# Kernel optimization log

Measured on AMD Instinct MI355X. Metric: run time of the kernel, lower is better.

## Reference

```python
import jax, jax.numpy as jnp
import numpy as np

EMBED = 768
HEADS = 12
HEAD_DIM = EMBED // HEADS
HIDDEN = 4 * EMBED
B, N = 8, 1024
EPS = 1e-5


def layernorm(x, g, b):
    mu = jnp.mean(x, axis=-1, keepdims=True)
    var = jnp.var(x, axis=-1, keepdims=True)
    return (x - mu) * jax.lax.rsqrt(var + EPS) * g + b


def setup_inputs() -> dict:
    key = jax.random.key(0)
    ks = jax.random.split(key, 8)
    s_qkv = 1.0 / np.sqrt(EMBED)
    s_fc1 = 1.0 / np.sqrt(EMBED)
    s_fc2 = 1.0 / np.sqrt(HIDDEN)
    return {
        "x": jax.random.normal(ks[0], (B, N, EMBED), dtype=jnp.float32),
        "ln1_g": jnp.ones((EMBED,), jnp.float32),
        "ln1_b": jnp.zeros((EMBED,), jnp.float32),
        "qkv_w": jax.random.uniform(ks[1], (3 * EMBED, EMBED), jnp.float32, -s_qkv, s_qkv),
        "qkv_b": jnp.zeros((3 * EMBED,), jnp.float32),
        "proj_w": jax.random.uniform(ks[2], (EMBED, EMBED), jnp.float32, -s_qkv, s_qkv),
        "proj_b": jnp.zeros((EMBED,), jnp.float32),
        "ln2_g": jnp.ones((EMBED,), jnp.float32),
        "ln2_b": jnp.zeros((EMBED,), jnp.float32),
        "fc1_w": jax.random.uniform(ks[3], (HIDDEN, EMBED), jnp.float32, -s_fc1, s_fc1),
        "fc1_b": jnp.zeros((HIDDEN,), jnp.float32),
        "fc2_w": jax.random.uniform(ks[4], (EMBED, HIDDEN), jnp.float32, -s_fc2, s_fc2),
        "fc2_b": jnp.zeros((EMBED,), jnp.float32),
    }


def reference(x, ln1_g, ln1_b, qkv_w, qkv_b, proj_w, proj_b,
              ln2_g, ln2_b, fc1_w, fc1_b, fc2_w, fc2_b):
    b, n, d = x.shape
    # --- attention sublayer ---
    h = layernorm(x, ln1_g, ln1_b)
    qkv = h @ qkv_w.T + qkv_b                      # [b,n,3d]
    qkv = qkv.reshape(b, n, 3, HEADS, HEAD_DIM).transpose(2, 0, 3, 1, 4)
    q, k, v = qkv[0], qkv[1], qkv[2]               # [b,h,n,hd]
    scores = jnp.einsum('bhqd,bhkd->bhqk', q, k) * (HEAD_DIM ** -0.5)
    attn = jax.nn.softmax(scores, axis=-1)
    ctx = jnp.einsum('bhqk,bhkd->bhqd', attn, v)   # [b,h,n,hd]
    ctx = ctx.transpose(0, 2, 1, 3).reshape(b, n, d)
    x = x + (ctx @ proj_w.T + proj_b)
    # --- MLP sublayer ---
    h = layernorm(x, ln2_g, ln2_b)
    h = jax.nn.gelu(h @ fc1_w.T + fc1_b, approximate=False)
    x = x + (h @ fc2_w.T + fc2_b)
    return x
```

## Files before the change

### kernel.cpp

```cpp
#include <hip/hip_runtime.h>
#include <cstdint>

typedef __bf16 bf16_t;
typedef __attribute__((ext_vector_type(8))) __bf16 bf16x8;
typedef __attribute__((ext_vector_type(4))) __bf16 bf16x4;
typedef __attribute__((ext_vector_type(4))) float f32x4;

#define MFMA16(a, b, c) __builtin_amdgcn_mfma_f32_16x16x32_bf16((a), (b), (c), 0, 0, 0)

#define GLOAD16(g, l) __builtin_amdgcn_global_load_lds(                      \
    (const __attribute__((address_space(1))) void*)(g),                      \
    (__attribute__((address_space(3))) void*)(l), 16, 0, 0)

__device__ inline float gelu_f(float v) {
    const float u = v + 0.044715f * v * v * v;
    return v / (1.0f + exp2f(-2.3022038f * u));
}

__global__ __launch_bounds__(256) void cvt4_kernel(const float* __restrict__ s0, bf16_t* __restrict__ d0,
                                                   const float* __restrict__ s1, bf16_t* __restrict__ d1,
                                                   const float* __restrict__ s2, bf16_t* __restrict__ d2,
                                                   const float* __restrict__ s3, bf16_t* __restrict__ d3) {
    const int blk = blockIdx.x;
    const float* s; bf16_t* d; int base;
    if (blk < 864)       { s = s0; d = d0; base = blk; }
    else if (blk < 1152) { s = s1; d = d1; base = blk - 864; }
    else if (blk < 2304) { s = s2; d = d2; base = blk - 1152; }
    else                 { s = s3; d = d3; base = blk - 2304; }
    const int i = (base * 256 + threadIdx.x) * 8;
    const float4* sp = (const float4*)(s + i);
    float4 a = sp[0], b = sp[1];
    bf16x8 o;
    o[0] = (bf16_t)a.x; o[1] = (bf16_t)a.y; o[2] = (bf16_t)a.z; o[3] = (bf16_t)a.w;
    o[4] = (bf16_t)b.x; o[5] = (bf16_t)b.y; o[6] = (bf16_t)b.z; o[7] = (bf16_t)b.w;
    *(bf16x8*)(d + i) = o;
}

__global__ __launch_bounds__(256) void ln_kernel(const float* __restrict__ x,
                                                 const float* __restrict__ gw,
                                                 const float* __restrict__ bw,
                                                 bf16_t* __restrict__ out) {
    const int row  = blockIdx.x * 4 + (threadIdx.x >> 6);
    const int lane = threadIdx.x & 63;
    const float4* xr = (const float4*)(x + (long)row * 768);
    float4 v[3];
    float s = 0.f, q = 0.f;
#pragma unroll
    for (int j = 0; j < 3; ++j) {
        v[j] = xr[j * 64 + lane];
        s += v[j].x + v[j].y + v[j].z + v[j].w;
        q += v[j].x * v[j].x + v[j].y * v[j].y + v[j].z * v[j].z + v[j].w * v[j].w;
    }
#pragma unroll
    for (int off = 32; off > 0; off >>= 1) {
        s += __shfl_xor(s, off);
        q += __shfl_xor(q, off);
    }
    const float mu = s * (1.0f / 768.0f);
    const float rs = rsqrtf(q * (1.0f / 768.0f) - mu * mu + 1e-5f);
#pragma unroll
    for (int j = 0; j < 3; ++j) {
        float4 g4 = ((const float4*)gw)[j * 64 + lane];
        float4 b4 = ((const float4*)bw)[j * 64 + lane];
        bf16x4 o;
        o[0] = (bf16_t)((v[j].x - mu) * rs * g4.x + b4.x);
        o[1] = (bf16_t)((v[j].y - mu) * rs * g4.y + b4.y);
        o[2] = (bf16_t)((v[j].z - mu) * rs * g4.z + b4.z);
        o[3] = (bf16_t)((v[j].w - mu) * rs * g4.w + b4.w);
        *(bf16x4*)(out + (long)row * 768 + (j * 64 + lane) * 4) = o;
    }
}

template <int MODE, int NC, int RPX>
__global__ __launch_bounds__(256) void gemm_bt(const bf16_t* __restrict__ A,
                                               const bf16_t* __restrict__ Bw,
                                               const float* __restrict__ bias,
                                               bf16_t* __restrict__ outb,
                                               bf16_t* __restrict__ o1,
                                               bf16_t* __restrict__ o2,
                                               int Nn, int K,
                                               const float* __restrict__ resf,
                                               float* __restrict__ outf) {
    __shared__ __align__(16) char smem[3 * (128 * 32 + 128 * 32) * 2];
    bf16_t* As = (bf16_t*)smem;
    bf16_t* Bs = (bf16_t*)(smem + 3 * 128 * 32 * 2);
    const int id = blockIdx.x;
    const int xcd = id & 7, sblk = id >> 3;
    const int tn = (sblk % NC) * 128;
    const int tm = (xcd * RPX + sblk / NC) * 128;
    const int w = threadIdx.x >> 6, l = threadIdx.x & 63;
    const int quad = l >> 4, r16 = l & 15;
    const int wm = (w >> 1) * 64, wn = (w & 1) * 64;
    f32x4 acc[4][4] = {};
    const bf16_t* ga = A  + (long)(tm + w * 32 + (l >> 2)) * K + (l & 3) * 8;
    const bf16_t* gb = Bw + (long)(tn + w * 32 + (l >> 2)) * K + (l & 3) * 8;
    const int lw = w * 1024;
    const int NK = K >> 5;

    auto issue = [&](int t) {
        const bf16_t* gan = ga + t * 32;
        const bf16_t* gbn = gb + t * 32;
        bf16_t* ab = As + (t % 3) * 4096;
        bf16_t* bb = Bs + (t % 3) * 4096;
        GLOAD16(gan,          ab + lw);
        GLOAD16(gan + 16 * K, ab + lw + 512);
        GLOAD16(gbn,          bb + lw);
        GLOAD16(gbn + 16 * K, bb + lw + 512);
    };
    auto compute = [&](int t) {
        const bf16_t* ab = As + (t % 3) * 4096;
        const bf16_t* bb = Bs + (t % 3) * 4096;
        bf16x8 af[4], bfr[4];
#pragma unroll
        for (int i = 0; i < 4; ++i) {
            af[i]  = *(const bf16x8*)&ab[(wm + i * 16 + r16) * 32 + quad * 8];
            bfr[i] = *(const bf16x8*)&bb[(wn + i * 16 + r16) * 32 + quad * 8];
        }
#pragma unroll
        for (int i = 0; i < 4; ++i)
#pragma unroll
            for (int j = 0; j < 4; ++j)
                acc[i][j] = MFMA16(af[i], bfr[j], acc[i][j]);
    };

    issue(0);
    issue(1);
    for (int t = 0; t < NK - 1; ++t) {
        asm volatile("s_waitcnt vmcnt(4)" ::: "memory");
        __builtin_amdgcn_s_barrier();
        if (t + 2 < NK) issue(t + 2);
        compute(t);
    }
    asm volatile("s_waitcnt vmcnt(0)" ::: "memory");
    __builtin_amdgcn_s_barrier();
    compute(NK - 1);

    __syncthreads();
    if (MODE == 3) {
        float* tf = (float*)smem + w * 16 * 68;
#pragma unroll
        for (int i = 0; i < 4; ++i) {
#pragma unroll
            for (int j = 0; j < 4; ++j) {
                const float bv = bias[tn + wn + j * 16 + r16];
#pragma unroll
                for (int rr = 0; rr < 4; ++rr)
                    tf[(quad * 4 + rr) * 68 + j * 16 + r16] = acc[i][j][rr] + bv;
            }
            const int grow = tm + wm + i * 16 + (l >> 2);
#pragma unroll
            for (int it = 0; it < 4; ++it) {
                const int gcol = tn + wn + (l & 3) * 4 + it * 16;
                f32x4 vv = *(const f32x4*)&tf[(l >> 2) * 68 + (l & 3) * 4 + it * 16];
                const float4 rv = *(const float4*)(resf + (long)grow * Nn + gcol);
                float4 ov;
                ov.x = rv.x + vv[0]; ov.y = rv.y + vv[1];
                ov.z = rv.z + vv[2]; ov.w = rv.w + vv[3];
                *(float4*)(outf + (long)grow * Nn + gcol) = ov;
            }
        }
        return;
    }
    bf16_t* tw = (bf16_t*)smem + w * 16 * 72;
    if (MODE == 0) {
        const int sect = (tn + wn) / 768;
        const int cwb  = tn + wn - sect * 768;
        const int h    = cwb >> 6;
        if (sect == 2) {
#pragma unroll
            for (int i = 0; i < 4; ++i) {
                const int r0 = tm + wm + i * 16 + quad * 4;
                const int b = r0 >> 10, n0 = r0 & 1023;
#pragma unroll
                for (int j = 0; j < 4; ++j) {
                    const int d = j * 16 + r16;
                    const float bv = bias[tn + wn + j * 16 + r16];
                    bf16_t* dst = o2 + ((long)(b * 12 + h) * 64 + d) * 1024;
#pragma unroll
                    for (int rr = 0; rr < 4; ++rr) {
                        const int nn = n0 + rr;
                        const int c = ((nn & 15) << 3) | ((nn >> 4) & 7);
                        dst[(nn & 0x380) + c] = (bf16_t)(acc[i][j][rr] + bv);
                    }
                }
            }
        } else {
            bf16_t* dstbuf = (sect == 0 ? outb : o1);
#pragma unroll
            for (int i = 0; i < 4; ++i) {
#pragma unroll
                for (int j = 0; j < 4; ++j) {
                    const float bv = bias[tn + wn + j * 16 + r16];
#pragma unroll
                    for (int rr = 0; rr < 4; ++rr)
                        tw[(quad * 4 + rr) * 72 + j * 16 + r16] = (bf16_t)(acc[i][j][rr] + bv);
                }
                const int tok = tm + wm + i * 16 + (l >> 2);
                const int b = tok >> 10, n0 = tok & 1023;
                const long base = (long)(b * 12 + h) * 65536 + (long)n0 * 64;
#pragma unroll
                for (int it = 0; it < 2; ++it) {
                    bf16x8 vv = *(const bf16x8*)&tw[(l >> 2) * 72 + (l & 3) * 8 + it * 32];
                    *(bf16x8*)(dstbuf + base + (l & 3) * 8 + it * 32) = vv;
                }
            }
        }
    } else {
#pragma unroll
        for (int i = 0; i < 4; ++i) {
#pragma unroll
            for (int j = 0; j < 4; ++j) {
                const float bv = bias[tn + wn + j * 16 + r16];
#pragma unroll
                for (int rr = 0; rr < 4; ++rr)
                    tw[(quad * 4 + rr) * 72 + j * 16 + r16] = (bf16_t)gelu_f(acc[i][j][rr] + bv);
            }
            const int grow = tm + wm + i * 16 + (l >> 2);
#pragma unroll
            for (int it = 0; it < 2; ++it) {
                bf16x8 vv = *(const bf16x8*)&tw[(l >> 2) * 72 + (l & 3) * 8 + it * 32];
                *(bf16x8*)(outb + (long)grow * Nn + tn + wn + (l & 3) * 8 + it * 32) = vv;
            }
        }
    }
}

__global__ __launch_bounds__(256, 3) void attn_kernel(const bf16_t* __restrict__ qh,
                                                      const bf16_t* __restrict__ kh,
                                                      const bf16_t* __restrict__ vt,
                                                      bf16_t* __restrict__ ctx) {
    __shared__ __align__(16) bf16_t Ks[128 * 72];
    __shared__ __align__(16) bf16_t Vt[64 * 136];
    __shared__ __align__(16) bf16_t Ps[4 * 16 * 136];
    const int w = threadIdx.x >> 6, l = threadIdx.x & 63;
    const int quad = l >> 4, r16 = l & 15;
    const int bh = blockIdx.x, qt = blockIdx.y;
    const bf16_t* qp = qh + (long)bh * 65536;
    const bf16_t* kp = kh + (long)bh * 65536;
    const bf16_t* vp = vt + (long)bh * 65536;
    const int q0 = qt * 128 + w * 32;
    const float SC = 0.18033688011f;

    bf16x8 qf[2][2];
#pragma unroll
    for (int mt = 0; mt < 2; ++mt)
#pragma unroll
        for (int kq = 0; kq < 2; ++kq)
            qf[mt][kq] = *(const bf16x8*)(qp + (long)(q0 + mt * 16 + r16) * 64 + kq * 32 + quad * 8);

    float lsum[2][4] = {};
    f32x4 oacc[2][4] = {};
    bf16_t* pw = Ps + w * 16 * 136;

    bf16x8 kpre[4], vpre[4];
#pragma unroll
    for (int c = 0; c < 4; ++c) {
        const int cc = threadIdx.x + c * 256;
        kpre[c] = *(const bf16x8*)(kp + (long)(cc >> 3) * 64 + (cc & 7) * 8);
        vpre[c] = *(const bf16x8*)(vp + (long)(cc >> 4) * 1024 + (cc & 15) * 8);
    }

    for (int kt = 0; kt < 8; ++kt) {
        __syncthreads();
#pragma unroll
        for (int c = 0; c < 4; ++c) {
            const int cc = threadIdx.x + c * 256;
            *(bf16x8*)&Ks[(cc >> 3) * 72 + (cc & 7) * 8] = kpre[c];
            *(bf16x8*)&Vt[(cc >> 4) * 136 + (cc & 15) * 8] = vpre[c];
        }
        __syncthreads();
        if (kt < 7) {
            const int kb = (kt + 1) * 128;
#pragma unroll
            for (int c = 0; c < 4; ++c) {
                const int cc = threadIdx.x + c * 256;
                kpre[c] = *(const bf16x8*)(kp + (long)(kb + (cc >> 3)) * 64 + (cc & 7) * 8);
                vpre[c] = *(const bf16x8*)(vp + (long)(cc >> 4) * 1024 + kb + (cc & 15) * 8);
            }
        }

#pragma unroll
        for (int mt = 0; mt < 2; ++mt) {
            f32x4 s[8] = {};
#pragma unroll
            for (int nt = 0; nt < 8; ++nt) {
                bf16x8 kf0 = *(const bf16x8*)&Ks[(nt * 16 + r16) * 72 + quad * 8];
                bf16x8 kf1 = *(const bf16x8*)&Ks[(nt * 16 + r16) * 72 + 32 + quad * 8];
                s[nt] = MFMA16(qf[mt][0], kf0, s[nt]);
                s[nt] = MFMA16(qf[mt][1], kf1, s[nt]);
            }
#pragma unroll
            for (int rr = 0; rr < 4; ++rr) {
                bf16x8 pv;
#pragma unroll
                for (int nt = 0; nt < 8; ++nt) {
                    const float p = exp2f(s[nt][rr] * SC);
                    lsum[mt][rr] += p;
                    pv[nt] = (bf16_t)p;
                }
                *(bf16x8*)&pw[(quad * 4 + rr) * 136 + r16 * 8] = pv;
            }
#pragma unroll
            for (int kc = 0; kc < 4; ++kc) {
                bf16x8 pf = *(const bf16x8*)&pw[r16 * 136 + kc * 32 + quad * 8];
#pragma unroll
                for (int dt = 0; dt < 4; ++dt) {
                    bf16x8 vf = *(const bf16x8*)&Vt[(dt * 16 + r16) * 136 + kc * 32 + quad * 8];
                    oacc[mt][dt] = MFMA16(pf, vf, oacc[mt][dt]);
                }
            }
        }
    }
#pragma unroll
    for (int mt = 0; mt < 2; ++mt)
#pragma unroll
        for (int rr = 0; rr < 4; ++rr) {
#pragma unroll
            for (int off = 1; off < 16; off <<= 1)
                lsum[mt][rr] += __shfl_xor(lsum[mt][rr], off);
        }
    const int b = bh / 12, h = bh % 12;
    const long tb = (long)b * 1024;
#pragma unroll
    for (int mt = 0; mt < 2; ++mt) {
#pragma unroll
        for (int dt = 0; dt < 4; ++dt)
#pragma unroll
            for (int rr = 0; rr < 4; ++rr)
                pw[(quad * 4 + rr) * 72 + dt * 16 + r16] =
                    (bf16_t)(oacc[mt][dt][rr] / lsum[mt][rr]);
        const int tok = q0 + mt * 16 + (l >> 2);
        const int off = (l & 3) * 16;
        bf16_t* dst = ctx + (tb + tok) * 768 + h * 64 + off;
        const bf16_t* src = &pw[(l >> 2) * 72 + off];
#pragma unroll
        for (int it = 0; it < 2; ++it)
            *(bf16x8*)(dst + it * 8) = *(const bf16x8*)(src + it * 8);
    }
}

extern "C" void kernel_launch(void* const* d_in, const int* in_sizes, int n_in,
                              void* d_out, int out_size, void* d_ws, size_t ws_size,
                              hipStream_t stream) {
    const float* x      = (const float*)d_in[0];
    const float* ln1_g  = (const float*)d_in[1];
    const float* ln1_b  = (const float*)d_in[2];
    const float* qkv_w  = (const float*)d_in[3];
    const float* qkv_b  = (const float*)d_in[4];
    const float* proj_w = (const float*)d_in[5];
    const float* proj_b = (const float*)d_in[6];
    const float* ln2_g  = (const float*)d_in[7];
    const float* ln2_b  = (const float*)d_in[8];
    const float* fc1_w  = (const float*)d_in[9];
    const float* fc1_b  = (const float*)d_in[10];
    const float* fc2_w  = (const float*)d_in[11];
    const float* fc2_b  = (const float*)d_in[12];

    char* p = (char*)d_ws;
    bf16_t* wqkv  = (bf16_t*)p; p += (size_t)2304 * 768 * 2;
    bf16_t* wproj = (bf16_t*)p; p += (size_t)768 * 768 * 2;
    bf16_t* wfc1  = (bf16_t*)p; p += (size_t)3072 * 768 * 2;
    bf16_t* wfc2  = (bf16_t*)p; p += (size_t)768 * 3072 * 2;
    bf16_t* h1    = (bf16_t*)p; p += (size_t)8192 * 768 * 2;
    bf16_t* qhb   = (bf16_t*)p; p += (size_t)96 * 1024 * 64 * 2;
    bf16_t* khb   = (bf16_t*)p; p += (size_t)96 * 1024 * 64 * 2;
    bf16_t* vtb   = (bf16_t*)p; p += (size_t)96 * 64 * 1024 * 2;
    bf16_t* ctx   = (bf16_t*)p; p += (size_t)8192 * 768 * 2;
    float*  x2    = (float*)p;  p += (size_t)8192 * 768 * 4;
    bf16_t* h2    = (bf16_t*)p; p += (size_t)8192 * 768 * 2;
    bf16_t* a1    = (bf16_t*)p; p += (size_t)8192 * 3072 * 2;

    cvt4_kernel<<<3456, 256, 0, stream>>>(qkv_w, wqkv, proj_w, wproj, fc1_w, wfc1, fc2_w, wfc2);

    ln_kernel<<<2048, 256, 0, stream>>>(x, ln1_g, ln1_b, h1);
    gemm_bt<0, 18, 8><<<1152, 256, 0, stream>>>(h1, wqkv, qkv_b, qhb, khb, vtb, 2304, 768,
                                                nullptr, nullptr);
    attn_kernel<<<dim3(96, 8), 256, 0, stream>>>(qhb, khb, vtb, ctx);
    gemm_bt<3, 6, 8><<<384, 256, 0, stream>>>(ctx, wproj, proj_b, nullptr, nullptr, nullptr,
                                              768, 768, x, x2);
    ln_kernel<<<2048, 256, 0, stream>>>(x2, ln2_g, ln2_b, h2);
    gemm_bt<2, 24, 8><<<1536, 256, 0, stream>>>(h2, wfc1, fc1_b, a1, nullptr, nullptr, 3072, 768,
                                                nullptr, nullptr);
    gemm_bt<3, 6, 8><<<384, 256, 0, stream>>>(a1, wfc2, fc2_b, nullptr, nullptr, nullptr,
                                              768, 3072, x2, (float*)d_out);
}
```

Before: 347.4 us.

## Add dedicated 256x256-tile FC1 GEMM with fused GELU and 4-stage LDS pipeline

Replaces the generic 128-tile FC1 GEMM with a specialized kernel using 256x256 output tiles, 512 threads, a 4-deep global_load_lds ring buffer with split-half MFMA scheduling and setprio, and XCD-aware tile mapping. The larger tile raises arithmetic intensity and cuts LDS/global traffic per FLOP. The bias+GELU epilogue is staged through LDS for coalesced 16-byte stores. The costs are heavy register pressure from 32 accumulators per lane, 128KB of LDS per block, and only 384 blocks, which may underfill the GPU.

```diff
diff --git a/kernel.cpp b/kernel.cpp
--- a/kernel.cpp
+++ b/kernel.cpp
@@ -68,6 +68,109 @@
         o[2] = (bf16_t)((v[j].z - mu) * rs * g4.z + b4.z);
         o[3] = (bf16_t)((v[j].w - mu) * rs * g4.w + b4.w);
         *(bf16x4*)(out + (long)row * 768 + (j * 64 + lane) * 4) = o;
+    }
+}
+
+__global__ __launch_bounds__(512, 2) void gemm256_gelu(const bf16_t* __restrict__ A,
+                                                       const bf16_t* __restrict__ Bw,
+                                                       const float* __restrict__ bias,
+                                                       bf16_t* __restrict__ outb) {
+    constexpr int K = 768, NK = 24, Nn = 3072;
+    __shared__ __align__(16) char smem[4 * 32768];
+    const int id = blockIdx.x;
+    const int xcd = id & 7, s = id >> 3;
+    const int tn = (s % 12) * 256;
+    const int tm = (xcd * 4 + s / 12) * 256;
+    const int tid = threadIdx.x;
+    const int wid = tid >> 6, l = tid & 63;
+    const int wr = wid >> 2, wc = wid & 3;
+    const int quad = l >> 4, r16 = l & 15;
+
+    const bf16_t* ga = A  + (long)(tm + wid * 32 + (l >> 2)) * K + (l & 3) * 8;
+    const bf16_t* gb = Bw + (long)(tn + wid * 32 + (l >> 2)) * K + (l & 3) * 8;
+
+    f32x4 acc[8][4] = {};
+    bf16x8 a[8], b[4];
+
+    auto abuf = [&](int t) { return (bf16_t*)(smem + (t & 3) * 32768); };
+    auto bbuf = [&](int t) { return (bf16_t*)(smem + (t & 3) * 32768 + 16384); };
+    auto issueA = [&](int t) {
+        bf16_t* d = abuf(t) + wid * 1024;
+        GLOAD16(ga + t * 32,          d);
+        GLOAD16(ga + 16 * K + t * 32, d + 512);
+    };
+    auto issueB = [&](int t) {
+        bf16_t* d = bbuf(t) + wid * 1024;
+        GLOAD16(gb + t * 32,          d);
+        GLOAD16(gb + 16 * K + t * 32, d + 512);
+    };
+    auto lda = [&](int t, int h) {
+        const bf16_t* p = abuf(t);
+#pragma unroll
+        for (int i = 0; i < 4; ++i)
+            a[h * 4 + i] = *(const bf16x8*)&p[(wr * 128 + (h * 4 + i) * 16 + r16) * 32 + quad * 8];
+    };
+    auto ldb = [&](int t) {
+        const bf16_t* p = bbuf(t);
+#pragma unroll
+        for (int j = 0; j < 4; ++j)
+            b[j] = *(const bf16x8*)&p[(wc * 64 + j * 16 + r16) * 32 + quad * 8];
+    };
+    auto mfma_half = [&](int h) {
+        __builtin_amdgcn_s_setprio(1);
+#pragma unroll
+        for (int i = 0; i < 4; ++i)
+#pragma unroll
+            for (int j = 0; j < 4; ++j)
+                acc[h * 4 + i][j] = MFMA16(a[h * 4 + i], b[j], acc[h * 4 + i][j]);
+        __builtin_amdgcn_s_setprio(0);
+    };
+
+    issueA(0); issueB(0);
+    issueA(1); issueB(1);
+    for (int t = 0; t < NK - 2; ++t) {
+        issueA(t + 2);
+        asm volatile("s_waitcnt vmcnt(6)" ::: "memory");
+        __builtin_amdgcn_s_barrier();
+        lda(t, 0); ldb(t);
+        mfma_half(0);
+        issueB(t + 2);
+        __builtin_amdgcn_s_barrier();
+        lda(t, 1);
+        mfma_half(1);
+    }
+    asm volatile("s_waitcnt vmcnt(4)" ::: "memory");
+    __builtin_amdgcn_s_barrier();
+    lda(NK - 2, 0); ldb(NK - 2);
+    mfma_half(0);
+    __builtin_amdgcn_s_barrier();
+    lda(NK - 2, 1);
+    mfma_half(1);
+    asm volatile("s_waitcnt vmcnt(0)" ::: "memory");
+    __builtin_amdgcn_s_barrier();
+    lda(NK - 1, 0); ldb(NK - 1);
+    mfma_half(0);
+    __builtin_amdgcn_s_barrier();
+    lda(NK - 1, 1);
+    mfma_half(1);
+
+    __syncthreads();
+    bf16_t* tw = (bf16_t*)smem + wid * 16 * 72;
+#pragma unroll
+    for (int i = 0; i < 8; ++i) {
+#pragma unroll
+        for (int j = 0; j < 4; ++j) {
+            const float bv = bias[tn + wc * 64 + j * 16 + r16];
+#pragma unroll
+            for (int rr = 0; rr < 4; ++rr)
+                tw[(quad * 4 + rr) * 72 + j * 16 + r16] = (bf16_t)gelu_f(acc[i][j][rr] + bv);
+        }
+        const int grow = tm + wr * 128 + i * 16 + (l >> 2);
+#pragma unroll
+        for (int it = 0; it < 2; ++it) {
+            bf16x8 vv = *(const bf16x8*)&tw[(l >> 2) * 72 + (l & 3) * 8 + it * 32];
+            *(bf16x8*)(outb + (long)grow * Nn + tn + wc * 64 + (l & 3) * 8 + it * 32) = vv;
+        }
     }
 }
 
@@ -379,8 +482,7 @@
     gemm_bt<3, 6, 8><<<384, 256, 0, stream>>>(ctx, wproj, proj_b, nullptr, nullptr, nullptr,
                                               768, 768, x, x2);
     ln_kernel<<<2048, 256, 0, stream>>>(x2, ln2_g, ln2_b, h2);
-    gemm_bt<2, 24, 8><<<1536, 256, 0, stream>>>(h2, wfc1, fc1_b, a1, nullptr, nullptr, 3072, 768,
-                                                nullptr, nullptr);
+    gemm256_gelu<<<384, 512, 0, stream>>>(h2, wfc1, fc1_b, a1);
     gemm_bt<3, 6, 8><<<384, 256, 0, stream>>>(a1, wfc2, fc2_b, nullptr, nullptr, nullptr,
                                               768, 3072, x2, (float*)d_out);
 }
```

Result: slower. 357.6 us (+2.9%).
